# Kernel optimization log

Measured on AMD Instinct MI355X. Metric: run time of the kernel, lower is better.

The kernel has to match this reference:

```python
import jax, jax.numpy as jnp
import numpy as np

B, T, F, H, C = 128, 512, 784, 256, 10
BN_EPS = 1e-3  # keras BatchNormalization default epsilon


def setup_inputs() -> dict:
    key = jax.random.key(0)
    ks = jax.random.split(key, 12)
    x = jax.random.normal(ks[0], (B, T, F), dtype=jnp.float32)
    # PeepholeLSTMCell params; keras gate order is [i, f, c, o]
    kernel = jax.random.normal(ks[1], (F, 4 * H), dtype=jnp.float32) / np.sqrt(F)
    rec_kernel = jax.random.normal(ks[2], (H, 4 * H), dtype=jnp.float32) / np.sqrt(H)
    bias = jnp.concatenate([
        jnp.zeros((H,), jnp.float32),   # i
        jnp.ones((H,), jnp.float32),    # f (unit_forget_bias=True)
        jnp.zeros((2 * H,), jnp.float32),  # c, o
    ])
    w_ci = jax.random.normal(ks[3], (H,), dtype=jnp.float32) * 0.1
    w_cf = jax.random.normal(ks[4], (H,), dtype=jnp.float32) * 0.1
    w_co = jax.random.normal(ks[5], (H,), dtype=jnp.float32) * 0.1
    # BatchNorm (inference-mode) params
    gamma = jnp.ones((H,), jnp.float32)
    beta = jnp.zeros((H,), jnp.float32)
    mov_mean = jax.random.normal(ks[6], (H,), dtype=jnp.float32) * 0.1
    mov_var = jax.random.uniform(ks[7], (H,), dtype=jnp.float32, minval=0.5, maxval=1.5)
    fc_w = jax.random.normal(ks[8], (H, C), dtype=jnp.float32) / np.sqrt(H)
    return {"x": x, "kernel": kernel, "rec_kernel": rec_kernel, "bias": bias,
            "w_ci": w_ci, "w_cf": w_cf, "w_co": w_co,
            "gamma": gamma, "beta": beta, "mov_mean": mov_mean, "mov_var": mov_var,
            "fc_w": fc_w}


def reference(x, kernel, rec_kernel, bias, w_ci, w_cf, w_co,
              gamma, beta, mov_mean, mov_var, fc_w):
    b, t, _ = x.shape
    h_dim = rec_kernel.shape[0]
    # Precompute input projection once (big GEMM): [B,T,4H]
    xw = jnp.einsum('btf,fk->btk', x, kernel) + bias

    def step(carry, xw_t):
        h, c = carry
        z = xw_t + h @ rec_kernel  # [B,4H]
        zi, zf, zc, zo = jnp.split(z, 4, axis=-1)
        i = jax.nn.sigmoid(zi + c * w_ci)        # input gate w/ peephole on c_prev
        f = jax.nn.sigmoid(zf + c * w_cf)        # forget gate w/ peephole on c_prev
        c_new = f * c + i * jnp.tanh(zc)
        o = jax.nn.sigmoid(zo + c_new * w_co)    # output gate w/ peephole on c_new
        h_new = o * jnp.tanh(c_new)
        return (h_new, c_new), h_new

    init = (jnp.zeros((b, h_dim), x.dtype), jnp.zeros((b, h_dim), x.dtype))
    _, hs = jax.lax.scan(step, init, xw.transpose(1, 0, 2))  # hs: [T,B,H]
    hs = hs.transpose(1, 0, 2).reshape(-1, h_dim)            # [B*T, H]
    # BN (inference) -> tanh -> bias-free Dense
    y = (hs - mov_mean) * jax.lax.rsqrt(mov_var + BN_EPS) * gamma + beta
    y = jnp.tanh(y)
    logits = y @ fc_w
    return logits.reshape(b, t, -1)
```

## Files before the change

### kernel.cpp

```cpp
#include <hip/hip_runtime.h>
#include <hip/hip_bf16.h>
#include <hip/hip_fp16.h>
#include <stdint.h>


typedef __attribute__((ext_vector_type(8))) short short8;
typedef __attribute__((ext_vector_type(4))) float f32x4;

__device__ __forceinline__ unsigned short f2bf(float f) {
  union { float f; uint32_t u; } v; v.f = f;
  return (unsigned short)((v.u + 0x7fffu + ((v.u >> 16) & 1u)) >> 16);
}
__device__ __forceinline__ float bfu2f(uint32_t u16) {
  union { uint32_t u; float f; } v; v.u = u16 << 16; return v.f;
}
__device__ __forceinline__ float sigm(float x) {
  return __builtin_amdgcn_rcpf(1.f + __expf(-x));
}
__device__ __forceinline__ float tanh_(float x) {
  float e = __expf(2.f * x);
  return 1.f - 2.f * __builtin_amdgcn_rcpf(e + 1.f);
}
__device__ __forceinline__ void bar_raw() {
  asm volatile("s_waitcnt lgkmcnt(0)" ::: "memory");
  __builtin_amdgcn_s_barrier();
  asm volatile("" ::: "memory");
}

__global__ void repack_w(const float* __restrict__ w, unsigned short* __restrict__ wt_hi,
                         unsigned short* __restrict__ wt_lo) {
  int idx = blockIdx.x * 256 + threadIdx.x;
  if (idx >= 1024 * 800) return;
  int n = idx / 800, k = idx - n * 800;
  float v = (k < 784) ? w[k * 1024 + n] : 0.f;
  unsigned short hi = f2bf(v);
  wt_hi[idx] = hi;
  wt_lo[idx] = f2bf(v - bfu2f(hi));
}

__global__ void repack_wf(const float* __restrict__ rk, unsigned short* __restrict__ wf) {
  int idx = blockIdx.x * 256 + threadIdx.x;
  if (idx >= 32768) return;
  int lane = idx & 63, ks = (idx >> 6) & 7, G = (idx >> 9) & 3;
  int w = (idx >> 11) & 3, g = (idx >> 13) & 3;
  int ncol = G * 256 + g * 64 + 16 * w + (lane & 15);
  int kb = ks * 32 + ((lane >> 4) << 3);
  union { unsigned short s[8]; uint4 v; } u;
  #pragma unroll
  for (int e = 0; e < 8; ++e) u.s[e] = f2bf(rk[(size_t)(kb + e) * 1024 + ncol]);
  ((uint4*)wf)[idx] = u.v;
}

__global__ __launch_bounds__(256, 2) void gemm_xw(
    const float* __restrict__ x, const unsigned short* __restrict__ wt_hi,
    const unsigned short* __restrict__ wt_lo, __half* __restrict__ xw) {
  __shared__ __align__(16) unsigned short As[128][40];
  __shared__ __align__(16) unsigned short Bh[128][40];
  __shared__ __align__(16) unsigned short Bl[128][40];
  const int tid = threadIdx.x;
  const int m0 = blockIdx.y << 7;
  const int n0 = blockIdx.x << 7;
  const int lane = tid & 63, wv = tid >> 6;
  const int wr = wv >> 1, wc = wv & 1;
  const int fm = lane & 15;
  const int fkb = (lane >> 4) << 3;
  const int sr = tid >> 1, sh = (tid & 1) << 4;
  f32x4 acc[4][4];
  #pragma unroll
  for (int a = 0; a < 4; ++a)
    #pragma unroll
    for (int b = 0; b < 4; ++b) acc[a][b] = (f32x4){0.f, 0.f, 0.f, 0.f};

  const float* xsrc = x + (size_t)(m0 + sr) * 784;
  const unsigned short* bhsrc = wt_hi + (size_t)(n0 + sr) * 800;
  const unsigned short* blsrc = wt_lo + (size_t)(n0 + sr) * 800;

  for (int kt = 0; kt < 25; ++kt) {
    const int kb = (kt << 5) + sh;
    float va[16];
    if (kb + 16 <= 784) {
      const float4* s = (const float4*)(xsrc + kb);
      #pragma unroll
      for (int q = 0; q < 4; ++q) {
        float4 f = s[q];
        va[q * 4 + 0] = f.x; va[q * 4 + 1] = f.y;
        va[q * 4 + 2] = f.z; va[q * 4 + 3] = f.w;
      }
    } else {
      #pragma unroll
      for (int q = 0; q < 16; ++q) va[q] = 0.f;
    }
    uint32_t pk[8];
    #pragma unroll
    for (int q = 0; q < 8; ++q)
      pk[q] = (uint32_t)f2bf(va[2 * q]) | ((uint32_t)f2bf(va[2 * q + 1]) << 16);
    uint4* adst = (uint4*)&As[sr][sh];
    adst[0] = make_uint4(pk[0], pk[1], pk[2], pk[3]);
    adst[1] = make_uint4(pk[4], pk[5], pk[6], pk[7]);
    const uint4* bh4 = (const uint4*)(bhsrc + kb);
    const uint4* bl4 = (const uint4*)(blsrc + kb);
    uint4* bhd = (uint4*)&Bh[sr][sh];
    uint4* bld = (uint4*)&Bl[sr][sh];
    bhd[0] = bh4[0]; bhd[1] = bh4[1];
    bld[0] = bl4[0]; bld[1] = bl4[1];
    __syncthreads();

    short8 af[4], bh[4], bl[4];
    #pragma unroll
    for (int mt = 0; mt < 4; ++mt)
      af[mt] = *(const short8*)&As[(wr << 6) + (mt << 4) + fm][fkb];
    #pragma unroll
    for (int nt = 0; nt < 4; ++nt) {
      bh[nt] = *(const short8*)&Bh[(wc << 6) + (nt << 4) + fm][fkb];
      bl[nt] = *(const short8*)&Bl[(wc << 6) + (nt << 4) + fm][fkb];
    }
    #pragma unroll
    for (int mt = 0; mt < 4; ++mt)
      #pragma unroll
      for (int nt = 0; nt < 4; ++nt) {
        acc[mt][nt] = __builtin_amdgcn_mfma_f32_16x16x32_bf16(af[mt], bh[nt], acc[mt][nt], 0, 0, 0);
        acc[mt][nt] = __builtin_amdgcn_mfma_f32_16x16x32_bf16(af[mt], bl[nt], acc[mt][nt], 0, 0, 0);
      }
    __syncthreads();
  }
  const int rbase = (lane >> 4) << 2;
  #pragma unroll
  for (int mt = 0; mt < 4; ++mt)
    #pragma unroll
    for (int nt = 0; nt < 4; ++nt) {
      int col = n0 + (wc << 6) + (nt << 4) + fm;
      #pragma unroll
      for (int r = 0; r < 4; ++r) {
        int row = m0 + (wr << 6) + (mt << 4) + rbase + r;
        xw[(size_t)row * 1024 + col] = __float2half(acc[mt][nt][r]);
      }
    }
}

__global__ __launch_bounds__(256, 1) void scan_kernel(
    const unsigned short* __restrict__ wf, __half* __restrict__ xw,
    unsigned long long* __restrict__ pub,
    const float* __restrict__ bias, const float* __restrict__ wci,
    const float* __restrict__ wcf, const float* __restrict__ wco,
    const float* __restrict__ gamma, const float* __restrict__ beta,
    const float* __restrict__ mean, const float* __restrict__ var) {
  __shared__ __align__(16) unsigned short h_all[16][264];
  __shared__ __align__(16) uint4 wlds[8192];
  const int tid = threadIdx.x, lane = tid & 63, w = tid >> 6;
  const int gr = blockIdx.x & 7;
  const int g = blockIdx.x >> 3;
  const int c = lane & 15, q = lane >> 4;
  const int jj = 16 * w + c, jg = 64 * g + jj;

  {
    const uint4* src = (const uint4*)wf + (size_t)g * 8192;
    for (int i = tid; i < 8192; i += 256) wlds[i] = src[i];
  }
  const short8* wl8 = (const short8*)wlds;

  const float b0 = bias[jg], b1 = bias[256 + jg], b2 = bias[512 + jg], b3 = bias[768 + jg];
  const float pci = wci[jg], pcf = wcf[jg], pco = wco[jg];
  const float bna = gamma[jg] * rsqrtf(var[jg] + 1e-3f);
  const float bnb = beta[jg] - mean[jg] * bna;
  float c2[4] = {0.f, 0.f, 0.f, 0.f};

  unsigned long long* mypub = pub + (size_t)(gr * 4 + g) * 512 + jj * 8 + q * 2;
  __hip_atomic_store(mypub + 0, 0ull, __ATOMIC_RELAXED, __HIP_MEMORY_SCOPE_SYSTEM);
  __hip_atomic_store(mypub + 1, 0ull, __ATOMIC_RELAXED, __HIP_MEMORY_SCOPE_SYSTEM);
  __hip_atomic_store(mypub + 16384, 0ull, __ATOMIC_RELAXED, __HIP_MEMORY_SCOPE_SYSTEM);
  __hip_atomic_store(mypub + 16385, 0ull, __ATOMIC_RELAXED, __HIP_MEMORY_SCOPE_SYSTEM);

  const unsigned long long* q0 = pub + (size_t)(gr * 4 + ((g + 1) & 3)) * 512 + 2 * tid;
  const unsigned long long* q1 = pub + (size_t)(gr * 4 + ((g + 2) & 3)) * 512 + 2 * tid;
  const unsigned long long* q2 = pub + (size_t)(gr * 4 + ((g + 3) & 3)) * 512 + 2 * tid;

  const size_t xbase = ((size_t)(gr * 16 + 4 * q) << 9);

  float xp[4][4];
  #pragma unroll
  for (int G = 0; G < 4; ++G)
    #pragma unroll
    for (int r = 0; r < 4; ++r)
      xp[G][r] = __half2float(xw[((xbase + ((size_t)r << 9)) << 10) + G * 256 + jg]);

  __syncthreads();

  for (int s = 0; s < 512; ++s) {
    f32x4 acc[4];
    #pragma unroll
    for (int G = 0; G < 4; ++G) acc[G] = (f32x4){0.f, 0.f, 0.f, 0.f};

    if (s > 0) {
      unsigned long long v0, v1, v2, v3, v4, v5;
      long cnt = 0;
      const size_t slot = (size_t)(s & 1) * 16384;
      const unsigned s32 = (unsigned)s;
      for (;;) {
        v0 = __hip_atomic_load(q0 + slot, __ATOMIC_RELAXED, __HIP_MEMORY_SCOPE_SYSTEM);
        v1 = __hip_atomic_load(q0 + slot + 1, __ATOMIC_RELAXED, __HIP_MEMORY_SCOPE_SYSTEM);
        v2 = __hip_atomic_load(q1 + slot, __ATOMIC_RELAXED, __HIP_MEMORY_SCOPE_SYSTEM);
        v3 = __hip_atomic_load(q1 + slot + 1, __ATOMIC_RELAXED, __HIP_MEMORY_SCOPE_SYSTEM);
        v4 = __hip_atomic_load(q2 + slot, __ATOMIC_RELAXED, __HIP_MEMORY_SCOPE_SYSTEM);
        v5 = __hip_atomic_load(q2 + slot + 1, __ATOMIC_RELAXED, __HIP_MEMORY_SCOPE_SYSTEM);
        bool ok = ((unsigned)(v0 >> 32) == s32) & ((unsigned)(v1 >> 32) == s32) &
                  ((unsigned)(v2 >> 32) == s32) & ((unsigned)(v3 >> 32) == s32) &
                  ((unsigned)(v4 >> 32) == s32) & ((unsigned)(v5 >> 32) == s32);
        if (ok) break;
        if (++cnt > (1L << 22)) break;
      }
      unsigned long long vv[6] = {v0, v1, v2, v3, v4, v5};
      #pragma unroll
      for (int pp = 0; pp < 3; ++pp) {
        int p = (g + 1 + pp) & 3;
        #pragma unroll
        for (int u2 = 0; u2 < 2; ++u2) {
          int wid = 2 * tid + u2;
          unsigned long long v = vv[pp * 2 + u2];
          int jj2 = wid >> 3, qq = (wid >> 1) & 3, uu = wid & 1;
          int m0 = 4 * qq + 2 * uu, col = 64 * p + jj2;
          h_all[m0][col] = (unsigned short)(v & 0xffffu);
          h_all[m0 + 1][col] = (unsigned short)((v >> 16) & 0xffffu);
        }
      }
      bar_raw();
      #pragma unroll
      for (int ks = 0; ks < 8; ++ks) {
        short8 afk = *(const short8*)&h_all[c][ks * 32 + q * 8];
        #pragma unroll
        for (int G = 0; G < 4; ++G) {
          short8 bfr = wl8[((w * 4 + G) * 8 + ks) * 64 + lane];
          acc[G] = __builtin_amdgcn_mfma_f32_16x16x32_bf16(afk, bfr, acc[G], 0, 0, 0);
        }
      }
      bar_raw();
    }

    float hn[4];
    #pragma unroll
    for (int r = 0; r < 4; ++r) {
      float z0 = acc[0][r] + b0 + xp[0][r];
      float z1 = acc[1][r] + b1 + xp[1][r];
      float z2 = acc[2][r] + b2 + xp[2][r];
      float z3 = acc[3][r] + b3 + xp[3][r];
      float ig = sigm(z0 + c2[r] * pci);
      float fg = sigm(z1 + c2[r] * pcf);
      float cn = fg * c2[r] + ig * tanh_(z2);
      float og = sigm(z3 + cn * pco);
      float h = og * tanh_(cn);
      c2[r] = cn;
      hn[r] = h;
      if ((r & 1) && s < 511) {
        unsigned long long pv =
            ((unsigned long long)(unsigned)(s + 1) << 32) |
            (unsigned long long)(((uint32_t)f2bf(hn[r - 1])) |
                                 ((uint32_t)f2bf(hn[r]) << 16));
        __hip_atomic_store(mypub + (size_t)((s + 1) & 1) * 16384 + (r >> 1), pv,
                           __ATOMIC_RELAXED, __HIP_MEMORY_SCOPE_SYSTEM);
      }
    }
    #pragma unroll
    for (int r = 0; r < 4; ++r) h_all[4 * q + r][jg] = f2bf(hn[r]);
    #pragma unroll
    for (int r = 0; r < 4; ++r) {
      float y = tanh_(hn[r] * bna + bnb);
      xw[((xbase + ((size_t)r << 9) + s) << 10) + jg] = __float2half(y);
    }
    if (s < 511) {
      #pragma unroll
      for (int G = 0; G < 4; ++G)
        #pragma unroll
        for (int r = 0; r < 4; ++r)
          xp[G][r] = __half2float(
              xw[((xbase + ((size_t)r << 9) + (s + 1)) << 10) + G * 256 + jg]);
    }
  }
}

__global__ __launch_bounds__(256) void final_fc(const __half* __restrict__ xw,
                                                const float* __restrict__ fcw,
                                                float* __restrict__ out) {
  const int tid = threadIdx.x, lane = tid & 63, w = tid >> 6;
  const int wid = blockIdx.x * 4 + w;
  float fw[4][10];
  #pragma unroll
  for (int q = 0; q < 4; ++q)
    #pragma unroll
    for (int c = 0; c < 10; ++c) fw[q][c] = fcw[(lane * 4 + q) * 10 + c];
  for (int it = 0; it < 128; ++it) {
    const int row = it * 512 + wid;
    uint2 u = *(const uint2*)(xw + ((size_t)row << 10) + lane * 4);
    const __half* hp = (const __half*)&u;
    float y0 = __half2float(hp[0]), y1 = __half2float(hp[1]);
    float y2 = __half2float(hp[2]), y3 = __half2float(hp[3]);
    float p[10];
    #pragma unroll
    for (int c = 0; c < 10; ++c)
      p[c] = y0 * fw[0][c] + y1 * fw[1][c] + y2 * fw[2][c] + y3 * fw[3][c];
    #pragma unroll
    for (int off = 1; off < 64; off <<= 1)
      #pragma unroll
      for (int c = 0; c < 10; ++c) p[c] += __shfl_xor(p[c], off, 64);
    if (lane == 0) {
      #pragma unroll
      for (int c = 0; c < 10; ++c) out[(size_t)row * 10 + c] = p[c];
    }
  }
}

extern "C" void kernel_launch(void* const* d_in, const int* in_sizes, int n_in,
                              void* d_out, int out_size, void* d_ws, size_t ws_size,
                              hipStream_t stream) {
  const float* x     = (const float*)d_in[0];
  const float* kw    = (const float*)d_in[1];
  const float* rk    = (const float*)d_in[2];
  const float* bias  = (const float*)d_in[3];
  const float* wci   = (const float*)d_in[4];
  const float* wcf   = (const float*)d_in[5];
  const float* wco   = (const float*)d_in[6];
  const float* gamma = (const float*)d_in[7];
  const float* beta  = (const float*)d_in[8];
  const float* mean  = (const float*)d_in[9];
  const float* var   = (const float*)d_in[10];
  const float* fcw   = (const float*)d_in[11];
  float* out = (float*)d_out;

  char* ws = (char*)d_ws;
  __half*         xw    = (__half*)ws;
  unsigned short* wt_hi = (unsigned short*)(ws + 134217728);
  unsigned short* wt_lo = (unsigned short*)(ws + 134217728 + 1638400);
  unsigned short* wfrag = (unsigned short*)(ws + 134217728 + 3276800);
  unsigned long long* pub = (unsigned long long*)(ws + 134217728);

  repack_w<<<dim3((1024 * 800 + 255) / 256), dim3(256), 0, stream>>>(kw, wt_hi, wt_lo);
  repack_wf<<<dim3(128), dim3(256), 0, stream>>>(rk, wfrag);
  gemm_xw<<<dim3(8, 512), dim3(256), 0, stream>>>(x, wt_hi, wt_lo, xw);
  scan_kernel<<<dim3(32), dim3(256), 0, stream>>>(wfrag, xw, pub, bias,
                                                  wci, wcf, wco, gamma, beta, mean, var);
  final_fc<<<dim3(128), dim3(256), 0, stream>>>(xw, fcw, out);
}
```

Measured before the change: 1.933 ms.

## Double-buffer LDS h tile and prefetch peer flags before publishing

The shared h tile is double-buffered by step parity, so the second barrier after the MFMA loop is removed. The next step's loads from peer publication slots are issued speculatively right after the gate math, before this block's own publish stores, so the first poll often succeeds without waiting. Stores are batched into two after all four rows. This removes one barrier per step and some polling latency. It relies on the parity buffering being race-free, and the early poll may read stale values that then require a retry.

```diff
diff --git a/kernel.cpp b/kernel.cpp
--- a/kernel.cpp
+++ b/kernel.cpp
@@ -26,6 +26,9 @@
   __builtin_amdgcn_s_barrier();
   asm volatile("" ::: "memory");
 }
+
+#define PUB_LD(p) __hip_atomic_load((p), __ATOMIC_RELAXED, __HIP_MEMORY_SCOPE_SYSTEM)
+#define PUB_ST(p, v) __hip_atomic_store((p), (v), __ATOMIC_RELAXED, __HIP_MEMORY_SCOPE_SYSTEM)
 
 __global__ void repack_w(const float* __restrict__ w, unsigned short* __restrict__ wt_hi,
                          unsigned short* __restrict__ wt_lo) {
@@ -144,7 +147,7 @@
     const float* __restrict__ wcf, const float* __restrict__ wco,
     const float* __restrict__ gamma, const float* __restrict__ beta,
     const float* __restrict__ mean, const float* __restrict__ var) {
-  __shared__ __align__(16) unsigned short h_all[16][264];
+  __shared__ __align__(16) unsigned short h_all[2][16][264];
   __shared__ __align__(16) uint4 wlds[8192];
   const int tid = threadIdx.x, lane = tid & 63, w = tid >> 6;
   const int gr = blockIdx.x & 7;
@@ -165,10 +168,10 @@
   float c2[4] = {0.f, 0.f, 0.f, 0.f};
 
   unsigned long long* mypub = pub + (size_t)(gr * 4 + g) * 512 + jj * 8 + q * 2;
-  __hip_atomic_store(mypub + 0, 0ull, __ATOMIC_RELAXED, __HIP_MEMORY_SCOPE_SYSTEM);
-  __hip_atomic_store(mypub + 1, 0ull, __ATOMIC_RELAXED, __HIP_MEMORY_SCOPE_SYSTEM);
-  __hip_atomic_store(mypub + 16384, 0ull, __ATOMIC_RELAXED, __HIP_MEMORY_SCOPE_SYSTEM);
-  __hip_atomic_store(mypub + 16385, 0ull, __ATOMIC_RELAXED, __HIP_MEMORY_SCOPE_SYSTEM);
+  PUB_ST(mypub + 0, 0ull);
+  PUB_ST(mypub + 1, 0ull);
+  PUB_ST(mypub + 16384, 0ull);
+  PUB_ST(mypub + 16385, 0ull);
 
   const unsigned long long* q0 = pub + (size_t)(gr * 4 + ((g + 1) & 3)) * 512 + 2 * tid;
   const unsigned long long* q1 = pub + (size_t)(gr * 4 + ((g + 2) & 3)) * 512 + 2 * tid;
@@ -185,27 +188,31 @@
 
   __syncthreads();
 
+  unsigned long long v0 = 0, v1 = 0, v2 = 0, v3 = 0, v4 = 0, v5 = 0;
+
   for (int s = 0; s < 512; ++s) {
+    const int par = s & 1;
     f32x4 acc[4];
     #pragma unroll
     for (int G = 0; G < 4; ++G) acc[G] = (f32x4){0.f, 0.f, 0.f, 0.f};
 
     if (s > 0) {
-      unsigned long long v0, v1, v2, v3, v4, v5;
+      const size_t slot = (size_t)par * 16384;
+      const unsigned s32 = (unsigned)s;
+      bool ok = ((unsigned)(v0 >> 32) == s32) & ((unsigned)(v1 >> 32) == s32) &
+                ((unsigned)(v2 >> 32) == s32) & ((unsigned)(v3 >> 32) == s32) &
+                ((unsigned)(v4 >> 32) == s32) & ((unsigned)(v5 >> 32) == s32);
       long cnt = 0;
-      const size_t slot = (size_t)(s & 1) * 16384;
-      const unsigned s32 = (unsigned)s;
-      for (;;) {
-        v0 = __hip_atomic_load(q0 + slot, __ATOMIC_RELAXED, __HIP_MEMORY_SCOPE_SYSTEM);
-        v1 = __hip_atomic_load(q0 + slot + 1, __ATOMIC_RELAXED, __HIP_MEMORY_SCOPE_SYSTEM);
-        v2 = __hip_atomic_load(q1 + slot, __ATOMIC_RELAXED, __HIP_MEMORY_SCOPE_SYSTEM);
-        v3 = __hip_atomic_load(q1 + slot + 1, __ATOMIC_RELAXED, __HIP_MEMORY_SCOPE_SYSTEM);
-        v4 = __hip_atomic_load(q2 + slot, __ATOMIC_RELAXED, __HIP_MEMORY_SCOPE_SYSTEM);
-        v5 = __hip_atomic_load(q2 + slot + 1, __ATOMIC_RELAXED, __HIP_MEMORY_SCOPE_SYSTEM);
-        bool ok = ((unsigned)(v0 >> 32) == s32) & ((unsigned)(v1 >> 32) == s32) &
-                  ((unsigned)(v2 >> 32) == s32) & ((unsigned)(v3 >> 32) == s32) &
-                  ((unsigned)(v4 >> 32) == s32) & ((unsigned)(v5 >> 32) == s32);
-        if (ok) break;
+      while (!ok) {
+        v0 = PUB_LD(q0 + slot);
+        v1 = PUB_LD(q0 + slot + 1);
+        v2 = PUB_LD(q1 + slot);
+        v3 = PUB_LD(q1 + slot + 1);
+        v4 = PUB_LD(q2 + slot);
+        v5 = PUB_LD(q2 + slot + 1);
+        ok = ((unsigned)(v0 >> 32) == s32) & ((unsigned)(v1 >> 32) == s32) &
+             ((unsigned)(v2 >> 32) == s32) & ((unsigned)(v3 >> 32) == s32) &
+             ((unsigned)(v4 >> 32) == s32) & ((unsigned)(v5 >> 32) == s32);
         if (++cnt > (1L << 22)) break;
       }
       unsigned long long vv[6] = {v0, v1, v2, v3, v4, v5};
@@ -218,21 +225,20 @@
           unsigned long long v = vv[pp * 2 + u2];
           int jj2 = wid >> 3, qq = (wid >> 1) & 3, uu = wid & 1;
           int m0 = 4 * qq + 2 * uu, col = 64 * p + jj2;
-          h_all[m0][col] = (unsigned short)(v & 0xffffu);
-          h_all[m0 + 1][col] = (unsigned short)((v >> 16) & 0xffffu);
+          h_all[par][m0][col] = (unsigned short)(v & 0xffffu);
+          h_all[par][m0 + 1][col] = (unsigned short)((v >> 16) & 0xffffu);
         }
       }
       bar_raw();
       #pragma unroll
       for (int ks = 0; ks < 8; ++ks) {
-        short8 afk = *(const short8*)&h_all[c][ks * 32 + q * 8];
+        short8 afk = *(const short8*)&h_all[par][c][ks * 32 + q * 8];
         #pragma unroll
         for (int G = 0; G < 4; ++G) {
           short8 bfr = wl8[((w * 4 + G) * 8 + ks) * 64 + lane];
           acc[G] = __builtin_amdgcn_mfma_f32_16x16x32_bf16(afk, bfr, acc[G], 0, 0, 0);
         }
       }
-      bar_raw();
     }
 
     float hn[4];
@@ -249,17 +255,29 @@
       float h = og * tanh_(cn);
       c2[r] = cn;
       hn[r] = h;
-      if ((r & 1) && s < 511) {
-        unsigned long long pv =
-            ((unsigned long long)(unsigned)(s + 1) << 32) |
-            (unsigned long long)(((uint32_t)f2bf(hn[r - 1])) |
-                                 ((uint32_t)f2bf(hn[r]) << 16));
-        __hip_atomic_store(mypub + (size_t)((s + 1) & 1) * 16384 + (r >> 1), pv,
-                           __ATOMIC_RELAXED, __HIP_MEMORY_SCOPE_SYSTEM);
-      }
-    }
-    #pragma unroll
-    for (int r = 0; r < 4; ++r) h_all[4 * q + r][jg] = f2bf(hn[r]);
+    }
+
+    if (s < 511) {
+      const size_t nslot = (size_t)((s + 1) & 1) * 16384;
+      v0 = PUB_LD(q0 + nslot);
+      v1 = PUB_LD(q0 + nslot + 1);
+      v2 = PUB_LD(q1 + nslot);
+      v3 = PUB_LD(q1 + nslot + 1);
+      v4 = PUB_LD(q2 + nslot);
+      v5 = PUB_LD(q2 + nslot + 1);
+      __builtin_amdgcn_sched_barrier(0);
+      unsigned long long pv0 =
+          ((unsigned long long)(unsigned)(s + 1) << 32) |
+          (unsigned long long)(((uint32_t)f2bf(hn[0])) | ((uint32_t)f2bf(hn[1]) << 16));
+      unsigned long long pv1 =
+          ((unsigned long long)(unsigned)(s + 1) << 32) |
+          (unsigned long long)(((uint32_t)f2bf(hn[2])) | ((uint32_t)f2bf(hn[3]) << 16));
+      PUB_ST(mypub + nslot + 0, pv0);
+      PUB_ST(mypub + nslot + 1, pv1);
+    }
+
+    #pragma unroll
+    for (int r = 0; r < 4; ++r) h_all[par ^ 1][4 * q + r][jg] = f2bf(hn[r]);
     #pragma unroll
     for (int r = 0; r < 4; ++r) {
       float y = tanh_(hn[r] * bna + bnb);
```

New measurement: 2.053 ms. 6.2% more time.
